# Performance work log

Hardware: AMD Instinct MI355X
Metric: run time of the kernel (lower is better)

Reference implementation:

```python
import jax, jax.numpy as jnp
import numpy as np

GATE_THRESH = 0.4
ALPHA_FN = lambda L: 1.0 - 1.0 / L  # length-adaptive alpha, called with actual L
EPS_NORM = 1e-12  # F.normalize eps
EPS_LN = 1e-5     # LayerNorm eps


def setup_inputs() -> dict:
    key = jax.random.key(0)
    B, L, H, V = 64, 2048, 128, 32000
    ks = jax.random.split(key, 8)
    s = lambda k, shape, fan: jax.random.normal(k, shape, jnp.float32) * (1.0 / np.sqrt(fan))
    return {
        "seq": jax.random.randint(ks[0], (B, L), 0, V, dtype=jnp.int64),
        "embed_w": jax.random.normal(ks[1], (V, H), jnp.float32) * 0.02,
        "ff_w1": s(ks[2], (2 * H, H), H), "ff_b1": jnp.zeros((2 * H,), jnp.float32),
        "ff_w2": s(ks[3], (H, 2 * H), 2 * H), "ff_b2": jnp.zeros((H,), jnp.float32),
        "ln_g": jnp.ones((H,), jnp.float32), "ln_b": jnp.zeros((H,), jnp.float32),
        "kp_w": s(ks[4], (H, H), H),
        "rp_w": s(ks[5], (H, H), H), "rp_b": jnp.zeros((H,), jnp.float32),
        "out_w": s(ks[6], (V, H), H), "out_b": jnpp if False else jnp.zeros((V,), jnp.float32),
    }


def reference(seq, embed_w, ff_w1, ff_b1, ff_w2, ff_b2, ln_g, ln_b, kp_w, rp_w, rp_b, out_w, out_b):
    h = embed_w[seq]                                            # [B,L,H]
    ff = jnp.maximum(h @ ff_w1.T + ff_b1, 0.0) @ ff_w2.T + ff_b2
    x = h + ff
    mu = x.mean(-1, keepdims=True)
    var = x.var(-1, keepdims=True)                              # biased, as LayerNorm
    h = (x - mu) / jnp.sqrt(var + EPS_LN) * ln_g + ln_b
    B, L, H = h.shape
    alpha = ALPHA_FN(L)
    k_all = jnp.einsum('blh,oh->blo', h, kp_w)                  # kp has no bias

    def step(M, k):                                             # M:[B,H,H], k:[B,H]
        kn = k / jnp.maximum(jnp.linalg.norm(k, axis=-1, keepdims=True), EPS_NORM)
        vp = jnp.einsum('bij,bj->bi', M, kn)
        d = k - vp
        delta = d[:, :, None] * kn[:, None, :]                  # outer product [B,H,H]
        fire = (jnp.linalg.norm(d, axis=-1) >= GATE_THRESH * jnp.linalg.norm(k, axis=-1)).astype(k.dtype)
        return M + (1.0 - alpha) * fire[:, None, None] * delta, None

    M0 = jnp.zeros((B, H, H), h.dtype)
    M, _ = jax.lax.scan(step, M0, jnp.swapaxes(k_all[:, :-1, :], 0, 1))  # scan over L-1 steps
    q = k_all[:, -1, :]
    read = jnp.einsum('bij,bj->bi', M, q)
    return (read @ rp_w.T + rp_b) @ out_w.T + out_b             # [B,V]
```

## Files before the change

kernel.cpp:

```cpp
#include <hip/hip_runtime.h>
#include <hip/hip_bf16.h>
#include <stdint.h>

#define Bn 64
#define Ln 2048
#define Hn 128
#define Vn 32000
#define THn 256
#define LAMBDA_ (1.0f/2048.0f)
#define CC 32
#define NCH (Ln/CC)
#define KP  132
#define VS  132
#define ADS 131
#define GS  36
#define GXS 33
#define MSR 36
#define MSW 576
#define HS  132

typedef short bf16x8 __attribute__((ext_vector_type(8)));
typedef float f32x4  __attribute__((ext_vector_type(4)));

__device__ __forceinline__ float rdlane(float v, int s) {
  return __int_as_float(__builtin_amdgcn_readlane(__float_as_int(v), s));
}

template <int CTRL>
__device__ __forceinline__ float dpp_add(float x) {
  int t = __builtin_amdgcn_update_dpp(0, __float_as_int(x), CTRL, 0xf, 0xf, false);
  return x + __int_as_float(t);
}
__device__ __forceinline__ float wave_sum64(float x) {
  x = dpp_add<0x111>(x);
  x = dpp_add<0x112>(x);
  x = dpp_add<0x114>(x);
  x = dpp_add<0x118>(x);
  x = dpp_add<0x142>(x);
  x = dpp_add<0x143>(x);
  return rdlane(x, 63);
}

__device__ __forceinline__ uint32_t packhl(float x) {
  uint32_t bx = __float_as_uint(x);
  float hf = __uint_as_float(bx & 0xFFFF0000u);
  uint32_t bl = __float_as_uint(x - hf);
  return (bx >> 16) | (bl & 0xFFFF0000u);
}
__device__ __forceinline__ float unpackhl(uint32_t u) {
  return __uint_as_float(u << 16) + __uint_as_float(u & 0xFFFF0000u);
}

struct FragHL { bf16x8 h; bf16x8 l; };
__device__ __forceinline__ FragHL mkfrag(const uint32_t* u) {
  union { uint32_t a[4]; bf16x8 v; } H, L;
  H.a[0] = __builtin_amdgcn_perm(u[1], u[0], 0x05040100u);
  H.a[1] = __builtin_amdgcn_perm(u[3], u[2], 0x05040100u);
  H.a[2] = __builtin_amdgcn_perm(u[5], u[4], 0x05040100u);
  H.a[3] = __builtin_amdgcn_perm(u[7], u[6], 0x05040100u);
  L.a[0] = __builtin_amdgcn_perm(u[1], u[0], 0x07060302u);
  L.a[1] = __builtin_amdgcn_perm(u[3], u[2], 0x07060302u);
  L.a[2] = __builtin_amdgcn_perm(u[5], u[4], 0x07060302u);
  L.a[3] = __builtin_amdgcn_perm(u[7], u[6], 0x07060302u);
  FragHL f; f.h = H.v; f.l = L.v; return f;
}

__device__ __forceinline__ void ld8(const uint32_t* p, uint32_t* u) {
  const uint4 a = *reinterpret_cast<const uint4*>(p);
  const uint4 b = *reinterpret_cast<const uint4*>(p + 4);
  u[0]=a.x; u[1]=a.y; u[2]=a.z; u[3]=a.w;
  u[4]=b.x; u[5]=b.y; u[6]=b.z; u[7]=b.w;
}

__device__ __forceinline__ bf16x8 asbf(uint4 u) {
  union { uint4 a; bf16x8 v; } c; c.a = u; return c.v;
}

__device__ __forceinline__ f32x4 mfma16(bf16x8 a, bf16x8 b, f32x4 c) {
  return __builtin_amdgcn_mfma_f32_16x16x32_bf16(a, b, c, 0, 0, 0);
}

__global__ __launch_bounds__(256) void p0_pack(
    const float* __restrict__ w1, const float* __restrict__ w2,
    const float* __restrict__ kp, uint32_t* __restrict__ wp)
{
  const int id = blockIdx.x*256 + threadIdx.x;
  const float* src; uint32_t *dh, *dl; int p;
  if (id < 16384)      { src = w1; p = id;         dh = wp;         dl = wp+16384; }
  else if (id < 32768) { src = w2; p = id-16384;   dh = wp+32768;   dl = wp+49152; }
  else                 { src = kp; p = id-32768;   dh = wp+65536;   dl = wp+73728; }
  const float x0 = src[2*p], x1 = src[2*p+1];
  const uint32_t b0 = __float_as_uint(x0), b1 = __float_as_uint(x1);
  const float l0f = x0 - __uint_as_float(b0 & 0xFFFF0000u);
  const float l1f = x1 - __uint_as_float(b1 & 0xFFFF0000u);
  dh[p] = (b0 >> 16) | ((b1 >> 16) << 16);
  dl[p] = (__float_as_uint(l0f) >> 16) | ((__float_as_uint(l1f) >> 16) << 16);
}

__global__ __launch_bounds__(256, 2) void p1_fused(
    const int* __restrict__ seq,
    const float* __restrict__ embed_w,
    const uint32_t* __restrict__ wp,
    const float* __restrict__ ff_b1, const float* __restrict__ ff_b2,
    const float* __restrict__ ln_g, const float* __restrict__ ln_b,
    uint32_t* __restrict__ knp_all, float* __restrict__ norm_all)
{
  __shared__ __align__(16) uint32_t h_p[64*HS];
  __shared__ __align__(16) uint32_t u_p[64*HS];
  __shared__ float part1[256], part2[256];
  __shared__ float mul[64], rsl[64];
  __shared__ int sid[64];

  const int tid  = threadIdx.x;
  const int lane = tid & 63;
  const int w    = __builtin_amdgcn_readfirstlane(tid >> 6);
  const int q4   = lane >> 4;
  const int m16  = lane & 15;
  const int tile0 = blockIdx.x * 64;

  const uint32_t* w1h = wp;
  const uint32_t* w1l = wp + 16384;
  const uint32_t* w2h = wp + 32768;
  const uint32_t* w2l = wp + 49152;
  const uint32_t* kph = wp + 65536;
  const uint32_t* kpl = wp + 73728;

  if (tid < 64) sid[tid] = seq[tile0 + tid];
  __syncthreads();

  {
    const int t = tid >> 2, part = tid & 3;
    const float4* erow =
        reinterpret_cast<const float4*>(embed_w + (size_t)sid[t]*Hn) + part*8;
    #pragma unroll
    for (int c = 0; c < 8; ++c) {
      float4 v = erow[c];
      int j = part*32 + c*4;
      h_p[t*HS+j+0] = packhl(v.x); h_p[t*HS+j+1] = packhl(v.y);
      h_p[t*HS+j+2] = packhl(v.z); h_p[t*HS+j+3] = packhl(v.w);
    }
  }
  __syncthreads();

  f32x4 acc2[4][2];
  #pragma unroll
  for (int tt=0;tt<4;++tt)
    #pragma unroll
    for (int ct=0;ct<2;++ct) acc2[tt][ct] = (f32x4){0.f,0.f,0.f,0.f};

  #pragma unroll 1
  for (int ho=0; ho<2; ++ho) {
    #pragma unroll 1
    for (int tt=0; tt<4; ++tt) {
      FragHL fa[4];
      #pragma unroll
      for (int kk=0;kk<4;++kk) {
        uint32_t ua[8];
        ld8(&h_p[(16*tt+m16)*HS + 32*kk + 8*q4], ua);
        fa[kk] = mkfrag(ua);
      }
      #pragma unroll
      for (int ct=0; ct<2; ++ct) {
        const int ob = 128*ho + 32*w + 16*ct;
        f32x4 a = (f32x4){0.f,0.f,0.f,0.f};
        #pragma unroll
        for (int kk=0;kk<4;++kk) {
          const size_t wi = (size_t)(ob+m16)*64 + 16*kk + 4*q4;
          bf16x8 bh = asbf(*reinterpret_cast<const uint4*>(&w1h[wi]));
          bf16x8 bl = asbf(*reinterpret_cast<const uint4*>(&w1l[wi]));
          a = mfma16(fa[kk].h, bh, a);
          a = mfma16(fa[kk].h, bl, a);
          a = mfma16(fa[kk].l, bh, a);
        }
        const float bb = ff_b1[ob + m16];
        #pragma unroll
        for (int reg=0;reg<4;++reg) {
          float uv = fmaxf(a[reg] + bb, 0.f);
          u_p[(16*tt+4*q4+reg)*HS + 32*w + 16*ct + m16] = packhl(uv);
        }
      }
    }
    __syncthreads();
    #pragma unroll 1
    for (int tt=0; tt<4; ++tt) {
      FragHL fu[4];
      #pragma unroll
      for (int kk=0;kk<4;++kk) {
        uint32_t ua[8];
        ld8(&u_p[(16*tt+m16)*HS + 32*kk + 8*q4], ua);
        fu[kk] = mkfrag(ua);
      }
      #pragma unroll
      for (int ct=0; ct<2; ++ct) {
        const int ib = 32*w + 16*ct;
        f32x4 a = acc2[tt][ct];
        #pragma unroll
        for (int kk=0;kk<4;++kk) {
          const size_t wi = (size_t)(ib+m16)*128 + 64*ho + 16*kk + 4*q4;
          bf16x8 bh = asbf(*reinterpret_cast<const uint4*>(&w2h[wi]));
          bf16x8 bl = asbf(*reinterpret_cast<const uint4*>(&w2l[wi]));
          a = mfma16(fu[kk].h, bh, a);
          a = mfma16(fu[kk].h, bl, a);
          a = mfma16(fu[kk].l, bh, a);
        }
        acc2[tt][ct] = a;
      }
    }
    __syncthreads();
  }

  float xx[4][2][4];
  #pragma unroll
  for (int tt=0;tt<4;++tt)
    #pragma unroll
    for (int ct=0;ct<2;++ct) {
      const int col = 32*w + 16*ct + m16;
      const float b2 = ff_b2[col];
      #pragma unroll
      for (int reg=0;reg<4;++reg) {
        const float hval = unpackhl(h_p[(16*tt+4*q4+reg)*HS + col]);
        xx[tt][ct][reg] = acc2[tt][ct][reg] + b2 + hval;
      }
    }
  #pragma unroll
  for (int tt=0;tt<4;++tt)
    #pragma unroll
    for (int reg=0;reg<4;++reg) {
      float s1 = xx[tt][0][reg] + xx[tt][1][reg];
      float s2 = xx[tt][0][reg]*xx[tt][0][reg] + xx[tt][1][reg]*xx[tt][1][reg];
      s1 += __shfl_xor(s1,1); s1 += __shfl_xor(s1,2);
      s1 += __shfl_xor(s1,4); s1 += __shfl_xor(s1,8);
      s2 += __shfl_xor(s2,1); s2 += __shfl_xor(s2,2);
      s2 += __shfl_xor(s2,4); s2 += __shfl_xor(s2,8);
      if (m16==0) {
        part1[w*64 + 16*tt+4*q4+reg] = s1;
        part2[w*64 + 16*tt+4*q4+reg] = s2;
      }
    }
  __syncthreads();
  if (tid < 64) {
    const float mu = (part1[tid]+part1[64+tid]+part1[128+tid]+part1[192+tid])*(1.0f/128.0f);
    const float ms = (part2[tid]+part2[64+tid]+part2[128+tid]+part2[192+tid])*(1.0f/128.0f);
    mul[tid] = mu;
    rsl[tid] = rsqrtf(ms - mu*mu + 1e-5f);
  }
  __syncthreads();

  #pragma unroll
  for (int tt=0;tt<4;++tt)
    #pragma unroll
    for (int ct=0;ct<2;++ct) {
      const int col = 32*w + 16*ct + m16;
      const float g = ln_g[col], bb = ln_b[col];
      #pragma unroll
      for (int reg=0;reg<4;++reg) {
        const int tok = 16*tt+4*q4+reg;
        const float hn = (xx[tt][ct][reg] - mul[tok])*rsl[tok]*g + bb;
        h_p[tok*HS + col] = packhl(hn);
      }
    }
  __syncthreads();

  f32x4 ak[4][2];
  #pragma unroll 1
  for (int tt=0;tt<4;++tt) {
    FragHL fh[4];
    #pragma unroll
    for (int kk=0;kk<4;++kk) {
      uint32_t ua[8];
      ld8(&h_p[(16*tt+m16)*HS + 32*kk + 8*q4], ua);
      fh[kk] = mkfrag(ua);
    }
    #pragma unroll
    for (int ct=0;ct<2;++ct) {
      const int ob = 32*w + 16*ct;
      f32x4 a = (f32x4){0.f,0.f,0.f,0.f};
      #pragma unroll
      for (int kk=0;kk<4;++kk) {
        const size_t wi = (size_t)(ob+m16)*64 + 16*kk + 4*q4;
        bf16x8 bh = asbf(*reinterpret_cast<const uint4*>(&kph[wi]));
        bf16x8 bl = asbf(*reinterpret_cast<const uint4*>(&kpl[wi]));
        a = mfma16(fh[kk].h, bh, a);
        a = mfma16(fh[kk].h, bl, a);
        a = mfma16(fh[kk].l, bh, a);
      }
      ak[tt][ct] = a;
    }
  }
  #pragma unroll
  for (int tt=0;tt<4;++tt)
    #pragma unroll
    for (int reg=0;reg<4;++reg) {
      float s = ak[tt][0][reg]*ak[tt][0][reg] + ak[tt][1][reg]*ak[tt][1][reg];
      s += __shfl_xor(s,1); s += __shfl_xor(s,2);
      s += __shfl_xor(s,4); s += __shfl_xor(s,8);
      if (m16==0) part1[w*64 + 16*tt+4*q4+reg] = s;
    }
  __syncthreads();
  if (tid < 64) {
    const float nn = part1[tid]+part1[64+tid]+part1[128+tid]+part1[192+tid];
    const float nrm = sqrtf(nn);
    norm_all[tile0 + tid] = nrm;
    mul[tid] = 1.0f / fmaxf(nrm, 1e-12f);
  }
  __syncthreads();
  #pragma unroll
  for (int tt=0;tt<4;++tt)
    #pragma unroll
    for (int ct=0;ct<2;++ct) {
      const int col = 32*w + 16*ct + m16;
      #pragma unroll
      for (int reg=0;reg<4;++reg) {
        const int tok = 16*tt+4*q4+reg;
        knp_all[(size_t)(tile0+tok)*Hn + col] = packhl(ak[tt][ct][reg]*mul[tok]);
      }
    }
}

__global__ __launch_bounds__(576, 1) void p2_scan(
    const uint32_t* __restrict__ knp_all, const float* __restrict__ norm_all,
    float* __restrict__ read_ws)
{
  const int tid  = threadIdx.x;
  const int lane = tid & 63;
  const int wv   = __builtin_amdgcn_readfirstlane(tid >> 6);
  const int q    = lane >> 4;
  const int m    = lane & 15;
  const int b    = blockIdx.x;

  __shared__ __align__(16) uint32_t kn_p[3*CC*KP];
  __shared__ __align__(16) float    vp0L[CC*VS];
  __shared__ __align__(16) float    adL [CC*ADS+4];
  __shared__ __align__(16) float    Gt  [2*CC*GS];
  __shared__ __align__(16) float    GxT [CC*GXS];
  __shared__ __align__(16) uint32_t msc [8*MSW];
  __shared__ float nrm_l[3*CC];

  f32x4 Macc[8];
  #pragma unroll
  for (int ct=0; ct<8; ++ct) Macc[ct] = (f32x4){0.f,0.f,0.f,0.f};

  const uint32_t* knb = knp_all + (size_t)b*Ln*Hn;
  const float*    nb  = norm_all + (size_t)b*Ln;

  {
    if (tid < 256) {
      const int t = tid>>3, g = tid&7;
      const uint4* src = reinterpret_cast<const uint4*>(knb + t*Hn + g*16);
      uint4* dst = reinterpret_cast<uint4*>(&kn_p[t*KP + g*16]);
      dst[0]=src[0]; dst[1]=src[1]; dst[2]=src[2]; dst[3]=src[3];
    } else if (tid < 512) {
      const int idx = tid-256, t = idx>>3, g = idx&7;
      const uint4* src = reinterpret_cast<const uint4*>(knb + CC*Hn + t*Hn + g*16);
      uint4* dst = reinterpret_cast<uint4*>(&kn_p[CC*KP + t*KP + g*16]);
      dst[0]=src[0]; dst[1]=src[1]; dst[2]=src[2]; dst[3]=src[3];
    } else {
      nrm_l[tid-512] = nb[tid-512];
    }
  }
  __syncthreads();

  {
    if (wv >= 5) {
      const int ti = (wv-5)>>1, si = (wv-5)&1;
      f32x4 g4 = (f32x4){0.f,0.f,0.f,0.f};
      #pragma unroll
      for (int kk=0; kk<4; ++kk) {
        uint32_t ua[8], ub[8];
        ld8(&kn_p[(16*ti+m)*KP + 32*kk + 8*q], ua);
        ld8(&kn_p[(16*si+m)*KP + 32*kk + 8*q], ub);
        FragHL fa = mkfrag(ua), fb = mkfrag(ub);
        g4 = mfma16(fa.h, fb.h, g4);
        g4 = mfma16(fa.h, fb.l, g4);
        g4 = mfma16(fa.l, fb.h, g4);
      }
      #pragma unroll
      for (int reg=0; reg<4; ++reg)
        Gt[(16*ti + 4*q + reg)*GS + 16*si + m] = g4[reg];
    }
    if (wv >= 1) {
      const int h0 = 16*(wv-1);
      const float nr0 = nrm_l[m], nr1 = nrm_l[16+m];
      const uint4 r0 = *reinterpret_cast<const uint4*>(&kn_p[m*KP + h0 + 4*q]);
      const uint4 r1 = *reinterpret_cast<const uint4*>(&kn_p[(16+m)*KP + h0 + 4*q]);
      const uint32_t* pr0 = &r0.x; const uint32_t* pr1 = &r1.x;
      #pragma unroll
      for (int reg=0; reg<4; ++reg) {
        const int h = h0 + 4*q + reg;
        vp0L[m*VS + h]      = nr0*unpackhl(pr0[reg]);
        vp0L[(16+m)*VS + h] = nr1*unpackhl(pr1[reg]);
      }
    }
  }
  __syncthreads();

  #pragma unroll 1
  for (int ch=0; ch<NCH; ++ch) {
    const int cur = ch%3, nx1 = (ch+1)%3, nx2 = (ch+2)%3;
    const int sel = ch & 1;
    const uint32_t* knc = &kn_p[cur*CC*KP];
    const uint32_t* knN = &kn_p[nx1*CC*KP];
    const bool havn  = (ch+1 < NCH);
    const bool havn2 = (ch+2 < NCH);

    uint4 pfa, pfb, pfc, pfd; float pfn = 0.f;
    if (havn2) {
      if (tid >= 320) {
        const int idx = tid-320, t = idx>>3, g = idx&7;
        const uint4* src = reinterpret_cast<const uint4*>(
            knb + (size_t)(ch+2)*CC*Hn + t*Hn + g*16);
        pfa=src[0]; pfb=src[1]; pfc=src[2]; pfd=src[3];
      }
      if (tid >= 288 && tid < 320) pfn = nb[(ch+2)*CC + (tid-288)];
    }

    f32x4 v0 = (f32x4){0.f,0.f,0.f,0.f};
    f32x4 v1 = (f32x4){0.f,0.f,0.f,0.f};

    if (wv==0) {
      float ad0[CC], ad1[CC], gr[CC];
      const float* GtS = &Gt[sel*CC*GS];
      #pragma unroll
      for (int t=0;t<CC;++t) gr[t] = GtS[t*GS + (lane&31)];
      const float nrmv = nrm_l[cur*CC + (lane&31)];
      #pragma unroll
      for (int t=0;t<CC;++t) {
        float a0c0 = vp0L[t*VS + lane];
        float a1c0 = vp0L[t*VS + 64 + lane];
        float a0c1=0.f, a0c2=0.f, a0c3=0.f;
        float a1c1=0.f, a1c2=0.f, a1c3=0.f;
        #pragma unroll
        for (int s=0; s<t; ++s) {
          const float g = rdlane(gr[t], s);
          switch (s & 3) {
            case 0: a0c0 -= g*ad0[s]; a1c0 -= g*ad1[s]; break;
            case 1: a0c1 -= g*ad0[s]; a1c1 -= g*ad1[s]; break;
            case 2: a0c2 -= g*ad0[s]; a1c2 -= g*ad1[s]; break;
            default:a0c3 -= g*ad0[s]; a1c3 -= g*ad1[s]; break;
          }
        }
        const float acc0 = (a0c0+a0c1)+(a0c2+a0c3);
        const float acc1 = (a1c0+a1c1)+(a1c2+a1c3);
        const float sqt = wave_sum64(acc0*acc0 + acc1*acc1);
        const float nrm = rdlane(nrmv, t);
        if (ch==NCH-1 && t==CC-1) {
          const float kn0 = unpackhl(knc[t*KP + lane]);
          const float kn1 = unpackhl(knc[t*KP + 64 + lane]);
          read_ws[b*Hn + lane]      = nrm*(nrm*kn0 - acc0);
          read_ws[b*Hn + 64 + lane] = nrm*(nrm*kn1 - acc1);
        } else {
          const float at = (sqt >= 0.16f*nrm*nrm) ? LAMBDA_ : 0.f;
          ad0[t] = at*acc0; ad1[t] = at*acc1;
          adL[t*ADS + lane]      = ad0[t];
          adL[t*ADS + 64 + lane] = ad1[t];
        }
      }
    } else {
      if (havn) {
        uint32_t* mybase = &msc[(wv-1)*MSW];
        #pragma unroll
        for (int kk=0; kk<4; ++kk) {
          #pragma unroll
          for (int c2=0; c2<2; ++c2) {
            const int ct = 2*kk + c2;
            #pragma unroll
            for (int reg=0; reg<4; ++reg)
              mybase[(4*q+reg)*MSR + 16*c2 + m] = packhl(Macc[ct][reg]);
          }
          uint32_t ua[8], ub[8];
          ld8(&mybase[m*MSR + 8*q], ua);
          FragHL fa = mkfrag(ua);
          ld8(&knN[m*KP + 32*kk + 8*q], ub);
          FragHL fb = mkfrag(ub);
          v0 = mfma16(fa.h, fb.h, v0);
          v0 = mfma16(fa.h, fb.l, v0);
          v0 = mfma16(fa.l, fb.h, v0);
          ld8(&knN[(16+m)*KP + 32*kk + 8*q], ub);
          fb = mkfrag(ub);
          v1 = mfma16(fa.h, fb.h, v1);
          v1 = mfma16(fa.h, fb.l, v1);
          v1 = mfma16(fa.l, fb.h, v1);
        }
        if (wv <= 4) {
          const int tj = (wv-1)>>1, ts = (wv-1)&1;
          f32x4 g4 = (f32x4){0.f,0.f,0.f,0.f};
          #pragma unroll
          for (int kk=0; kk<4; ++kk) {
            uint32_t ua[8], ub[8];
            ld8(&knN[(16*tj+m)*KP + 32*kk + 8*q], ua);
            ld8(&knc[(16*ts+m)*KP + 32*kk + 8*q], ub);
            FragHL fa = mkfrag(ua), fb = mkfrag(ub);
            g4 = mfma16(fa.h, fb.h, g4);
            g4 = mfma16(fa.h, fb.l, g4);
            g4 = mfma16(fa.l, fb.h, g4);
          }
          #pragma unroll
          for (int reg=0; reg<4; ++reg)
            GxT[(16*tj + 4*q + reg)*GXS + 16*ts + m] = g4[reg];
        } else {
          const int ti = (wv-5)>>1, si = (wv-5)&1;
          f32x4 g4 = (f32x4){0.f,0.f,0.f,0.f};
          #pragma unroll
          for (int kk=0; kk<4; ++kk) {
            uint32_t ua[8], ub[8];
            ld8(&knN[(16*ti+m)*KP + 32*kk + 8*q], ua);
            ld8(&knN[(16*si+m)*KP + 32*kk + 8*q], ub);
            FragHL fa = mkfrag(ua), fb = mkfrag(ub);
            g4 = mfma16(fa.h, fb.h, g4);
            g4 = mfma16(fa.h, fb.l, g4);
            g4 = mfma16(fa.l, fb.h, g4);
          }
          #pragma unroll
          for (int reg=0; reg<4; ++reg)
            Gt[(1-sel)*CC*GS + (16*ti + 4*q + reg)*GS + 16*si + m] = g4[reg];
        }
      }
      if (havn2) {
        if (tid >= 320) {
          const int idx = tid-320, t = idx>>3, g = idx&7;
          uint4* dst = reinterpret_cast<uint4*>(
              &kn_p[nx2*CC*KP + t*KP + g*16]);
          dst[0]=pfa; dst[1]=pfb; dst[2]=pfc; dst[3]=pfd;
        }
        if (tid >= 288 && tid < 320) nrm_l[nx2*CC + (tid-288)] = pfn;
      }
    }
    __syncthreads();
    if (ch==NCH-1) break;

    if (wv >= 1) {
      const int h0 = 16*(wv-1);
      {
        uint32_t ap[8];
        #pragma unroll
        for (int j=0;j<8;++j)
          ap[j] = packhl(adL[(8*q+j)*ADS + h0 + m]);
        FragHL fa = mkfrag(ap);
        #pragma unroll
        for (int ct=0; ct<8; ++ct) {
          uint32_t bu[8];
          #pragma unroll
          for (int j=0;j<8;++j)
            bu[j] = knc[(8*q+j)*KP + 16*ct + m];
          FragHL fb = mkfrag(bu);
          Macc[ct] = mfma16(fa.h, fb.h, Macc[ct]);
          Macc[ct] = mfma16(fa.h, fb.l, Macc[ct]);
          Macc[ct] = mfma16(fa.l, fb.h, Macc[ct]);
        }
      }
      f32x4 c0 = (f32x4){0.f,0.f,0.f,0.f};
      f32x4 c1 = (f32x4){0.f,0.f,0.f,0.f};
      {
        uint32_t* mybase = &msc[(wv-1)*MSW];
        #pragma unroll
        for (int c2=0; c2<2; ++c2)
          #pragma unroll
          for (int reg=0; reg<4; ++reg)
            mybase[(4*q+reg)*MSR + 16*c2 + m] =
                packhl(adL[(16*c2+m)*ADS + h0 + 4*q + reg]);
        uint32_t ua[8], gb[8];
        ld8(&mybase[m*MSR + 8*q], ua);
        FragHL fa = mkfrag(ua);
        #pragma unroll
        for (int jj=0;jj<8;++jj) gb[jj] = packhl(GxT[m*GXS + 8*q + jj]);
        FragHL fb = mkfrag(gb);
        c0 = mfma16(fa.h, fb.h, c0);
        c0 = mfma16(fa.h, fb.l, c0);
        c0 = mfma16(fa.l, fb.h, c0);
        #pragma unroll
        for (int jj=0;jj<8;++jj) gb[jj] = packhl(GxT[(16+m)*GXS + 8*q + jj]);
        fb = mkfrag(gb);
        c1 = mfma16(fa.h, fb.h, c1);
        c1 = mfma16(fa.h, fb.l, c1);
        c1 = mfma16(fa.l, fb.h, c1);
      }
      {
        const float nr0 = nrm_l[nx1*CC + m];
        const float nr1 = nrm_l[nx1*CC + 16 + m];
        const uint4 r0 = *reinterpret_cast<const uint4*>(&knN[m*KP + h0 + 4*q]);
        const uint4 r1 = *reinterpret_cast<const uint4*>(&knN[(16+m)*KP + h0 + 4*q]);
        const uint32_t* pr0 = &r0.x; const uint32_t* pr1 = &r1.x;
        #pragma unroll
        for (int reg=0; reg<4; ++reg) {
          const int h = h0 + 4*q + reg;
          vp0L[m*VS + h]      = nr0*unpackhl(pr0[reg]) - v0[reg] - c0[reg];
          vp0L[(16+m)*VS + h] = nr1*unpackhl(pr1[reg]) - v1[reg] - c1[reg];
        }
      }
    }
    __syncthreads();
  }
}

__global__ __launch_bounds__(128) void p3a(
    const float* __restrict__ read_ws, const float* __restrict__ rp_w,
    const float* __restrict__ rp_b, float* __restrict__ o1_ws)
{
  __shared__ float rd[128];
  const int b = blockIdx.x, t = threadIdx.x;
  rd[t] = read_ws[b*Hn + t];
  __syncthreads();
  float acc = rp_b[t];
  const float* wr = rp_w + t*Hn;
  #pragma unroll 4
  for (int i = 0; i < Hn; ++i) acc += rd[i]*wr[i];
  o1_ws[b*Hn + t] = acc;
}

__global__ __launch_bounds__(256) void p3b(
    const float* __restrict__ o1_ws, const float* __restrict__ out_w,
    const float* __restrict__ out_b, float* __restrict__ out)
{
  __shared__ __align__(16) float o1[8192];
  const int tid = threadIdx.x;
  #pragma unroll
  for (int c = 0; c < 32; ++c) o1[c*256+tid] = o1_ws[c*256+tid];
  __syncthreads();
  const int v = blockIdx.x*256 + tid;
  float acc[64];
  const float ob = out_b[v];
  #pragma unroll
  for (int bb = 0; bb < 64; ++bb) acc[bb] = ob;
  const float4* wrow = reinterpret_cast<const float4*>(out_w + (size_t)v*Hn);
  #pragma unroll 1
  for (int r4 = 0; r4 < 32; ++r4) {
    const float4 wv = wrow[r4];
    #pragma unroll
    for (int bb = 0; bb < 64; ++bb) {
      const float4 ov = *reinterpret_cast<const float4*>(&o1[bb*Hn + r4*4]);
      acc[bb] += wv.x*ov.x + wv.y*ov.y + wv.z*ov.z + wv.w*ov.w;
    }
  }
  #pragma unroll
  for (int bb = 0; bb < 64; ++bb) out[(size_t)bb*Vn + v] = acc[bb];
}

extern "C" void kernel_launch(void* const* d_in, const int* in_sizes, int n_in,
                              void* d_out, int out_size, void* d_ws, size_t ws_size,
                              hipStream_t stream)
{
  const int*   seq     = (const int*)  d_in[0];
  const float* embed_w = (const float*)d_in[1];
  const float* ff_w1   = (const float*)d_in[2];
  const float* ff_b1   = (const float*)d_in[3];
  const float* ff_w2   = (const float*)d_in[4];
  const float* ff_b2   = (const float*)d_in[5];
  const float* ln_g    = (const float*)d_in[6];
  const float* ln_b    = (const float*)d_in[7];
  const float* kp_w    = (const float*)d_in[8];
  const float* rp_w    = (const float*)d_in[9];
  const float* rp_b    = (const float*)d_in[10];
  const float* out_w   = (const float*)d_in[11];
  const float* out_b   = (const float*)d_in[12];

  float* ws          = (float*)d_ws;
  uint32_t* knp_all  = (uint32_t*)ws;
  float* norm_all    = ws + (size_t)Bn*Ln*Hn;
  float* read_ws     = norm_all + (size_t)Bn*Ln;
  float* o1_ws       = read_ws + Bn*Hn;
  uint32_t* wp       = (uint32_t*)(o1_ws + Bn*Hn);

  p0_pack<<<dim3(160), dim3(256), 0, stream>>>(ff_w1, ff_w2, kp_w, wp);
  p1_fused<<<dim3(2048), dim3(256), 0, stream>>>(
      seq, embed_w, wp, ff_b1, ff_b2, ln_g, ln_b, knp_all, norm_all);
  p2_scan<<<dim3(64), dim3(576), 0, stream>>>(knp_all, norm_all, read_ws);
  p3a<<<dim3(64), dim3(128), 0, stream>>>(read_ws, rp_w, rp_b, o1_ws);
  p3b<<<dim3(125), dim3(256), 0, stream>>>(o1_ws, out_w, out_b, (float*)d_out);
}
```

Measured before the change: 721.8 us.

## Defer M update into wave-0 phase and XOR-swizzle kn LDS layout

Result: slower. 888.1 us (+23.0%).

```diff
diff --git a/kernel.cpp b/kernel.cpp
--- a/kernel.cpp
+++ b/kernel.cpp
@@ -13,6 +13,7 @@
 #define KP  132
 #define VS  132
 #define ADS 131
+#define ADW (CC*ADS+4)
 #define GS  36
 #define GXS 33
 #define MSR 36
@@ -330,7 +331,7 @@
 
   __shared__ __align__(16) uint32_t kn_p[3*CC*KP];
   __shared__ __align__(16) float    vp0L[CC*VS];
-  __shared__ __align__(16) float    adL [CC*ADS+4];
+  __shared__ __align__(16) float    adL [2*ADW];
   __shared__ __align__(16) float    Gt  [2*CC*GS];
   __shared__ __align__(16) float    GxT [CC*GXS];
   __shared__ __align__(16) uint32_t msc [8*MSW];
@@ -343,17 +344,28 @@
   const uint32_t* knb = knp_all + (size_t)b*Ln*Hn;
   const float*    nb  = norm_all + (size_t)b*Ln;
 
+  const int swm  = ((m>>3)&3)<<3;
+  const int swm2 = (((16+m)>>3)&3)<<3;
+
   {
     if (tid < 256) {
       const int t = tid>>3, g = tid&7;
+      const int sw = ((t>>3)&3)<<3;
       const uint4* src = reinterpret_cast<const uint4*>(knb + t*Hn + g*16);
-      uint4* dst = reinterpret_cast<uint4*>(&kn_p[t*KP + g*16]);
-      dst[0]=src[0]; dst[1]=src[1]; dst[2]=src[2]; dst[3]=src[3];
+      uint32_t* dstb = &kn_p[t*KP];
+      *reinterpret_cast<uint4*>(&dstb[(16*g+0) ^ sw])  = src[0];
+      *reinterpret_cast<uint4*>(&dstb[(16*g+4) ^ sw])  = src[1];
+      *reinterpret_cast<uint4*>(&dstb[(16*g+8) ^ sw])  = src[2];
+      *reinterpret_cast<uint4*>(&dstb[(16*g+12) ^ sw]) = src[3];
     } else if (tid < 512) {
       const int idx = tid-256, t = idx>>3, g = idx&7;
+      const int sw = ((t>>3)&3)<<3;
       const uint4* src = reinterpret_cast<const uint4*>(knb + CC*Hn + t*Hn + g*16);
-      uint4* dst = reinterpret_cast<uint4*>(&kn_p[CC*KP + t*KP + g*16]);
-      dst[0]=src[0]; dst[1]=src[1]; dst[2]=src[2]; dst[3]=src[3];
+      uint32_t* dstb = &kn_p[CC*KP + t*KP];
+      *reinterpret_cast<uint4*>(&dstb[(16*g+0) ^ sw])  = src[0];
+      *reinterpret_cast<uint4*>(&dstb[(16*g+4) ^ sw])  = src[1];
+      *reinterpret_cast<uint4*>(&dstb[(16*g+8) ^ sw])  = src[2];
+      *reinterpret_cast<uint4*>(&dstb[(16*g+12) ^ sw]) = src[3];
     } else {
       nrm_l[tid-512] = nb[tid-512];
     }
@@ -363,12 +375,14 @@
   {
     if (wv >= 5) {
       const int ti = (wv-5)>>1, si = (wv-5)&1;
+      const int ra = 16*ti+m, rb = 16*si+m;
+      const int swa = ((ra>>3)&3)<<3, swb = ((rb>>3)&3)<<3;
       f32x4 g4 = (f32x4){0.f,0.f,0.f,0.f};
       #pragma unroll
       for (int kk=0; kk<4; ++kk) {
         uint32_t ua[8], ub[8];
-        ld8(&kn_p[(16*ti+m)*KP + 32*kk + 8*q], ua);
-        ld8(&kn_p[(16*si+m)*KP + 32*kk + 8*q], ub);
+        ld8(&kn_p[ra*KP + ((32*kk + 8*q) ^ swa)], ua);
+        ld8(&kn_p[rb*KP + ((32*kk + 8*q) ^ swb)], ub);
         FragHL fa = mkfrag(ua), fb = mkfrag(ub);
         g4 = mfma16(fa.h, fb.h, g4);
         g4 = mfma16(fa.h, fb.l, g4);
@@ -381,8 +395,8 @@
     if (wv >= 1) {
       const int h0 = 16*(wv-1);
       const float nr0 = nrm_l[m], nr1 = nrm_l[16+m];
-      const uint4 r0 = *reinterpret_cast<const uint4*>(&kn_p[m*KP + h0 + 4*q]);
-      const uint4 r1 = *reinterpret_cast<const uint4*>(&kn_p[(16+m)*KP + h0 + 4*q]);
+      const uint4 r0 = *reinterpret_cast<const uint4*>(&kn_p[m*KP + ((h0 + 4*q) ^ swm)]);
+      const uint4 r1 = *reinterpret_cast<const uint4*>(&kn_p[(16+m)*KP + ((h0 + 4*q) ^ swm2)]);
       const uint32_t* pr0 = &r0.x; const uint32_t* pr1 = &r1.x;
       #pragma unroll
       for (int reg=0; reg<4; ++reg) {
@@ -400,6 +414,7 @@
     const int sel = ch & 1;
     const uint32_t* knc = &kn_p[cur*CC*KP];
     const uint32_t* knN = &kn_p[nx1*CC*KP];
+    const uint32_t* knP = &kn_p[nx2*CC*KP];
     const bool havn  = (ch+1 < NCH);
     const bool havn2 = (ch+2 < NCH);
 
@@ -419,6 +434,7 @@
 
     if (wv==0) {
       float ad0[CC], ad1[CC], gr[CC];
+      float* adW = &adL[sel*ADW];
       const float* GtS = &Gt[sel*CC*GS];
       #pragma unroll
       for (int t=0;t<CC;++t) gr[t] = GtS[t*GS + (lane&31)];
@@ -444,19 +460,40 @@
         const float sqt = wave_sum64(acc0*acc0 + acc1*acc1);
         const float nrm = rdlane(nrmv, t);
         if (ch==NCH-1 && t==CC-1) {
-          const float kn0 = unpackhl(knc[t*KP + lane]);
-          const float kn1 = unpackhl(knc[t*KP + 64 + lane]);
+          const int swt = ((t>>3)&3)<<3;
+          const float kn0 = unpackhl(knc[t*KP + (lane ^ swt)]);
+          const float kn1 = unpackhl(knc[t*KP + ((64+lane) ^ swt)]);
           read_ws[b*Hn + lane]      = nrm*(nrm*kn0 - acc0);
           read_ws[b*Hn + 64 + lane] = nrm*(nrm*kn1 - acc1);
         } else {
           const float at = (sqt >= 0.16f*nrm*nrm) ? LAMBDA_ : 0.f;
           ad0[t] = at*acc0; ad1[t] = at*acc1;
-          adL[t*ADS + lane]      = ad0[t];
-          adL[t*ADS + 64 + lane] = ad1[t];
-        }
-      }
-    } else {
-      if (havn) {
+          adW[t*ADS + lane]      = ad0[t];
+          adW[t*ADS + 64 + lane] = ad1[t];
+        }
+      }
+    } else if (havn) {
+      const int h0 = 16*(wv-1);
+      if (ch >= 1) {
+        const float* adR = &adL[(1-sel)*ADW];
+        uint32_t ap[8];
+        #pragma unroll
+        for (int j=0;j<8;++j)
+          ap[j] = packhl(adR[(8*q+j)*ADS + h0 + m]);
+        FragHL fa = mkfrag(ap);
+        #pragma unroll
+        for (int ct=0; ct<8; ++ct) {
+          uint32_t bu[8];
+          #pragma unroll
+          for (int j=0;j<8;++j)
+            bu[j] = knP[(8*q+j)*KP + ((16*ct+m) ^ (q<<3))];
+          FragHL fb = mkfrag(bu);
+          Macc[ct] = mfma16(fa.h, fb.h, Macc[ct]);
+          Macc[ct] = mfma16(fa.h, fb.l, Macc[ct]);
+          Macc[ct] = mfma16(fa.l, fb.h, Macc[ct]);
+        }
+      }
+      {
         uint32_t* mybase = &msc[(wv-1)*MSW];
         #pragma unroll
         for (int kk=0; kk<4; ++kk) {
@@ -470,59 +507,54 @@
           uint32_t ua[8], ub[8];
           ld8(&mybase[m*MSR + 8*q], ua);
           FragHL fa = mkfrag(ua);
-          ld8(&knN[m*KP + 32*kk + 8*q], ub);
+          ld8(&knN[m*KP + ((32*kk + 8*q) ^ swm)], ub);
           FragHL fb = mkfrag(ub);
           v0 = mfma16(fa.h, fb.h, v0);
           v0 = mfma16(fa.h, fb.l, v0);
           v0 = mfma16(fa.l, fb.h, v0);
-          ld8(&knN[(16+m)*KP + 32*kk + 8*q], ub);
+          ld8(&knN[(16+m)*KP + ((32*kk + 8*q) ^ swm2)], ub);
           fb = mkfrag(ub);
           v1 = mfma16(fa.h, fb.h, v1);
           v1 = mfma16(fa.h, fb.l, v1);
           v1 = mfma16(fa.l, fb.h, v1);
         }
-        if (wv <= 4) {
-          const int tj = (wv-1)>>1, ts = (wv-1)&1;
-          f32x4 g4 = (f32x4){0.f,0.f,0.f,0.f};
-          #pragma unroll
-          for (int kk=0; kk<4; ++kk) {
-            uint32_t ua[8], ub[8];
-            ld8(&knN[(16*tj+m)*KP + 32*kk + 8*q], ua);
-            ld8(&knc[(16*ts+m)*KP + 32*kk + 8*q], ub);
-            FragHL fa = mkfrag(ua), fb = mkfrag(ub);
-            g4 = mfma16(fa.h, fb.h, g4);
-            g4 = mfma16(fa.h, fb.l, g4);
-            g4 = mfma16(fa.l, fb.h, g4);
-          }
-          #pragma unroll
-          for (int reg=0; reg<4; ++reg)
-            GxT[(16*tj + 4*q + reg)*GXS + 16*ts + m] = g4[reg];
-        } else {
-          const int ti = (wv-5)>>1, si = (wv-5)&1;
-          f32x4 g4 = (f32x4){0.f,0.f,0.f,0.f};
-          #pragma unroll
-          for (int kk=0; kk<4; ++kk) {
-            uint32_t ua[8], ub[8];
-            ld8(&knN[(16*ti+m)*KP + 32*kk + 8*q], ua);
-            ld8(&knN[(16*si+m)*KP + 32*kk + 8*q], ub);
-            FragHL fa = mkfrag(ua), fb = mkfrag(ub);
-            g4 = mfma16(fa.h, fb.h, g4);
-            g4 = mfma16(fa.h, fb.l, g4);
-            g4 = mfma16(fa.l, fb.h, g4);
-          }
-          #pragma unroll
-          for (int reg=0; reg<4; ++reg)
-            Gt[(1-sel)*CC*GS + (16*ti + 4*q + reg)*GS + 16*si + m] = g4[reg];
-        }
-      }
-      if (havn2) {
-        if (tid >= 320) {
-          const int idx = tid-320, t = idx>>3, g = idx&7;
-          uint4* dst = reinterpret_cast<uint4*>(
-              &kn_p[nx2*CC*KP + t*KP + g*16]);
-          dst[0]=pfa; dst[1]=pfb; dst[2]=pfc; dst[3]=pfd;
-        }
-        if (tid >= 288 && tid < 320) nrm_l[nx2*CC + (tid-288)] = pfn;
+      }
+      if (wv <= 4) {
+        const int tj = (wv-1)>>1, ts = (wv-1)&1;
+        const int ra = 16*tj+m, rb = 16*ts+m;
+        const int swa = ((ra>>3)&3)<<3, swb = ((rb>>3)&3)<<3;
+        f32x4 g4 = (f32x4){0.f,0.f,0.f,0.f};
+        #pragma unroll
+        for (int kk=0; kk<4; ++kk) {
+          uint32_t ua[8], ub[8];
+          ld8(&knN[ra*KP + ((32*kk + 8*q) ^ swa)], ua);
+          ld8(&knc[rb*KP + ((32*kk + 8*q) ^ swb)], ub);
+          FragHL fa = mkfrag(ua), fb = mkfrag(ub);
+          g4 = mfma16(fa.h, fb.h, g4);
+          g4 = mfma16(fa.h, fb.l, g4);
+          g4 = mfma16(fa.l, fb.h, g4);
+        }
+        #pragma unroll
+        for (int reg=0; reg<4; ++reg)
+          GxT[(16*tj + 4*q + reg)*GXS + 16*ts + m] = g4[reg];
+      } else {
+        const int ti = (wv-5)>>1, si = (wv-5)&1;
+        const int ra = 16*ti+m, rb = 16*si+m;
+        const int swa = ((ra>>3)&3)<<3, swb = ((rb>>3)&3)<<3;
+        f32x4 g4 = (f32x4){0.f,0.f,0.f,0.f};
+        #pragma unroll
+        for (int kk=0; kk<4; ++kk) {
+          uint32_t ua[8], ub[8];
+          ld8(&knN[ra*KP + ((32*kk + 8*q) ^ swa)], ua);
+          ld8(&knN[rb*KP + ((32*kk + 8*q) ^ swb)], ub);
+          FragHL fa = mkfrag(ua), fb = mkfrag(ub);
+          g4 = mfma16(fa.h, fb.h, g4);
+          g4 = mfma16(fa.h, fb.l, g4);
+          g4 = mfma16(fa.l, fb.h, g4);
+        }
+        #pragma unroll
+        for (int reg=0; reg<4; ++reg)
+          Gt[(1-sel)*CC*GS + (16*ti + 4*q + reg)*GS + 16*si + m] = g4[reg];
       }
     }
     __syncthreads();
@@ -530,34 +562,17 @@
 
     if (wv >= 1) {
       const int h0 = 16*(wv-1);
-      {
-        uint32_t ap[8];
-        #pragma unroll
-        for (int j=0;j<8;++j)
-          ap[j] = packhl(adL[(8*q+j)*ADS + h0 + m]);
-        FragHL fa = mkfrag(ap);
-        #pragma unroll
-        for (int ct=0; ct<8; ++ct) {
-          uint32_t bu[8];
-          #pragma unroll
-          for (int j=0;j<8;++j)
-            bu[j] = knc[(8*q+j)*KP + 16*ct + m];
-          FragHL fb = mkfrag(bu);
-          Macc[ct] = mfma16(fa.h, fb.h, Macc[ct]);
-          Macc[ct] = mfma16(fa.h, fb.l, Macc[ct]);
-          Macc[ct] = mfma16(fa.l, fb.h, Macc[ct]);
-        }
-      }
       f32x4 c0 = (f32x4){0.f,0.f,0.f,0.f};
       f32x4 c1 = (f32x4){0.f,0.f,0.f,0.f};
       {
+        const float* adR = &adL[sel*ADW];
         uint32_t* mybase = &msc[(wv-1)*MSW];
         #pragma unroll
         for (int c2=0; c2<2; ++c2)
           #pragma unroll
           for (int reg=0; reg<4; ++reg)
             mybase[(4*q+reg)*MSR + 16*c2 + m] =
-                packhl(adL[(16*c2+m)*ADS + h0 + 4*q + reg]);
+                packhl(adR[(16*c2+m)*ADS + h0 + 4*q + reg]);
         uint32_t ua[8], gb[8];
         ld8(&mybase[m*MSR + 8*q], ua);
         FragHL fa = mkfrag(ua);
@@ -577,8 +592,8 @@
       {
         const float nr0 = nrm_l[nx1*CC + m];
         const float nr1 = nrm_l[nx1*CC + 16 + m];
-        const uint4 r0 = *reinterpret_cast<const uint4*>(&knN[m*KP + h0 + 4*q]);
-        const uint4 r1 = *reinterpret_cast<const uint4*>(&knN[(16+m)*KP + h0 + 4*q]);
+        const uint4 r0 = *reinterpret_cast<const uint4*>(&knN[m*KP + ((h0 + 4*q) ^ swm)]);
+        const uint4 r1 = *reinterpret_cast<const uint4*>(&knN[(16+m)*KP + ((h0 + 4*q) ^ swm2)]);
         const uint32_t* pr0 = &r0.x; const uint32_t* pr1 = &r1.x;
         #pragma unroll
         for (int reg=0; reg<4; ++reg) {
@@ -586,6 +601,18 @@
           vp0L[m*VS + h]      = nr0*unpackhl(pr0[reg]) - v0[reg] - c0[reg];
           vp0L[(16+m)*VS + h] = nr1*unpackhl(pr1[reg]) - v1[reg] - c1[reg];
         }
+      }
+      if (havn2) {
+        if (tid >= 320) {
+          const int idx = tid-320, t = idx>>3, g = idx&7;
+          const int sw = ((t>>3)&3)<<3;
+          uint32_t* dstb = &kn_p[nx2*CC*KP + t*KP];
+          *reinterpret_cast<uint4*>(&dstb[(16*g+0) ^ sw])  = pfa;
+          *reinterpret_cast<uint4*>(&dstb[(16*g+4) ^ sw])  = pfb;
+          *reinterpret_cast<uint4*>(&dstb[(16*g+8) ^ sw])  = pfc;
+          *reinterpret_cast<uint4*>(&dstb[(16*g+12) ^ sw]) = pfd;
+        }
+        if (tid >= 288 && tid < 320) nrm_l[nx2*CC + (tid-288)] = pfn;
       }
     }
     __syncthreads();
```
